# Kernel tuning notes

Hardware: AMD Instinct MI355X
Metric: run time of the kernel (lower is better)

The kernel has to match this reference:

```python
import jax, jax.numpy as jnp
import numpy as np

N_NODES = 100000


def gcn_conv(x, W, b, edge_index, n):
    # GCNConv: x' = D^{-1/2}(A+I)D^{-1/2} (x W) + b  (self-loops added, symmetric norm)
    h = x @ W                                  # [n, out]
    loop = jnp.arange(n, dtype=edge_index.dtype)
    row = jnp.concatenate([edge_index[0], loop])
    col = jnp.concatenate([edge_index[1], loop])
    deg = jax.ops.segment_sum(jnp.ones(col.shape, h.dtype), col, num_segments=n)
    dinv = jnp.where(deg > 0, jax.lax.rsqrt(deg), 0.0)
    norm = dinv[row] * dinv[col]               # [E+n]
    out = jax.ops.segment_sum(norm[:, None] * h[row], col, num_segments=n)
    return out + b


def setup_inputs() -> dict:
    key = jax.random.key(0)
    k1, k2, k3, k4, k5 = jax.random.split(key, 5)
    N, F, H, O = N_NODES, 128, 64, 32
    E, EL = 3200000, 200000
    x = jax.random.normal(k1, (N, F), dtype=jnp.float32)
    W1 = jax.random.normal(k2, (F, H), dtype=jnp.float32) * (1.0 / np.sqrt(F))
    b1 = jnp.zeros((H,), dtype=jnp.float32)
    W2 = jax.random.normal(k3, (H, O), dtype=jnp.float32) * (1.0 / np.sqrt(H))
    b2 = jnp.zeros((O,), dtype=jnp.float32)
    edge_index = jax.random.randint(k4, (2, E), 0, N, dtype=jnp.int64)
    edge_label_index = jax.random.randint(k5, (2, EL), 0, N, dtype=jnp.int64)
    return {"x": x, "W1": W1, "b1": b1, "W2": W2, "b2": b2,
            "edge_index": edge_index, "edge_label_index": edge_label_index}


def reference(x, W1, b1, W2, b2, edge_index, edge_label_index):
    n = x.shape[0]
    z = gcn_conv(x, W1, b1, edge_index, n)
    z = jax.nn.relu(z)
    z = gcn_conv(z, W2, b2, edge_index, n)     # [n, 32]
    # dot-product link decode
    return (z[edge_label_index[0]] * z[edge_label_index[1]]).sum(axis=1)
```

## Files before the change

kernel.cpp:

```cpp
#include <hip/hip_runtime.h>
#include <hip/hip_bf16.h>

typedef __hip_bfloat16 bf16;
typedef short s8v __attribute__((ext_vector_type(8)));
typedef float f4v __attribute__((ext_vector_type(4)));
typedef float v2f __attribute__((ext_vector_type(2)));

__device__ __forceinline__ short f2b(float f) {
  bf16 h = __float2bfloat16(f);
  return *reinterpret_cast<short*>(&h);
}
__device__ __forceinline__ void bf2_acc(int d, v2f& a) {
  v2f u;
  u.x = __int_as_float(d << 16);
  u.y = __int_as_float(d & 0xFFFF0000);
  a += u;
}

#define BSHIFT 8
#define BNODES 256
#define CHUNK 4096
#define SORT_CAP 12288
#define TSHIFT 15

__global__ __launch_bounds__(256) void k_hist(const int* __restrict__ col, int E,
                                              int nbuck, int* __restrict__ chist) {
  __shared__ int hist[512];
  int t = threadIdx.x;
  hist[t] = 0; hist[t + 256] = 0;
  __syncthreads();
  int e0 = blockIdx.x * CHUNK;
#pragma unroll
  for (int i = 0; i < 16; i++) {
    int e = e0 + i * 256 + t;
    if (e < E) atomicAdd(&hist[col[e] >> BSHIFT], 1);
  }
  __syncthreads();
  int* out = chist + (size_t)blockIdx.x * nbuck;
  for (int b = t; b < nbuck; b += 256) out[b] = hist[b];
}

__global__ __launch_bounds__(256) void k_scanbuck(int* __restrict__ chist, int nchnk,
                                                  int nbuck, int* __restrict__ btot) {
  __shared__ int sm[256];
  int b = blockIdx.x, t = threadIdx.x;
  int per = (nchnk + 255) / 256;
  int lo = t * per, hi = min(lo + per, nchnk);
  int s = 0;
  for (int i = lo; i < hi; i++) s += chist[(size_t)i * nbuck + b];
  sm[t] = s;
  __syncthreads();
  for (int d = 1; d < 256; d <<= 1) {
    int x = (t >= d) ? sm[t - d] : 0;
    __syncthreads();
    sm[t] += x;
    __syncthreads();
  }
  int off = (t == 0) ? 0 : sm[t - 1];
  for (int i = lo; i < hi; i++) {
    int c = chist[(size_t)i * nbuck + b];
    chist[(size_t)i * nbuck + b] = off;
    off += c;
  }
  if (t == 255) btot[b] = sm[255];
}

__global__ __launch_bounds__(512) void k_scanbase(const int* __restrict__ btot, int nbuck,
                                                  int* __restrict__ bbase,
                                                  int* __restrict__ row_start, int n) {
  __shared__ int sm[512];
  int t = threadIdx.x;
  int v = (t < nbuck) ? btot[t] : 0;
  sm[t] = v;
  __syncthreads();
  for (int d = 1; d < 512; d <<= 1) {
    int x = (t >= d) ? sm[t - d] : 0;
    __syncthreads();
    sm[t] += x;
    __syncthreads();
  }
  if (t < nbuck) bbase[t] = sm[t] - v;
  if (t == nbuck - 1) {
    bbase[nbuck] = sm[t];
    row_start[n] = sm[t];
  }
}

__global__ __launch_bounds__(256) void k_binpass(const int* __restrict__ row,
                                                 const int* __restrict__ col, int E,
                                                 int nbuck,
                                                 const int* __restrict__ bbase,
                                                 const int* __restrict__ chist,
                                                 int* __restrict__ adjTmp) {
  __shared__ int hist[512];
  __shared__ int base[512];
  __shared__ int lcur[512];
  __shared__ int gbase[512];
  __shared__ int psum[256];
  __shared__ int stage[CHUNK];
  __shared__ unsigned short sbkt[CHUNK];
  __shared__ int s_total;
  int t = threadIdx.x;
  int e0 = blockIdx.x * CHUNK;

  hist[t] = 0; hist[t + 256] = 0;
  __syncthreads();

  int pk[16], bk[16];
#pragma unroll
  for (int i = 0; i < 16; i++) {
    int e = e0 + i * 256 + t;
    if (e < E) {
      int c = col[e];
      int r = row[e];
      bk[i] = c >> BSHIFT;
      pk[i] = r | ((c & (BNODES - 1)) << 17);
      atomicAdd(&hist[bk[i]], 1);
    } else bk[i] = -1;
  }
  __syncthreads();
  int a0 = hist[2 * t], a1 = hist[2 * t + 1];
  psum[t] = a0 + a1;
  __syncthreads();
  for (int d = 1; d < 256; d <<= 1) {
    int v = (t >= d) ? psum[t - d] : 0;
    __syncthreads();
    psum[t] += v;
    __syncthreads();
  }
  int pref = (t == 0) ? 0 : psum[t - 1];
  base[2 * t] = pref;          lcur[2 * t] = pref;
  base[2 * t + 1] = pref + a0; lcur[2 * t + 1] = pref + a0;
  if (t == 255) s_total = psum[255];
  const int* coff = chist + (size_t)blockIdx.x * nbuck;
  for (int b = t; b < nbuck; b += 256) gbase[b] = bbase[b] + coff[b];
  __syncthreads();
#pragma unroll
  for (int i = 0; i < 16; i++) {
    if (bk[i] >= 0) {
      int pos = atomicAdd(&lcur[bk[i]], 1);
      stage[pos] = pk[i];
      sbkt[pos] = (unsigned short)bk[i];
    }
  }
  __syncthreads();
  int total = s_total;
  for (int i = t; i < total; i += 256) {
    int b = sbkt[i];
    adjTmp[gbase[b] + (i - base[b])] = stage[i];
  }
}

__global__ __launch_bounds__(256) void k_bucketsort(const int* __restrict__ bbase,
                                                    const int* __restrict__ adjTmp,
                                                    int* __restrict__ adj,
                                                    int* __restrict__ row_start,
                                                    float* __restrict__ dinv, int n) {
  __shared__ int cnt[1024];
  __shared__ int sc[256];
  __shared__ int cur[1024];
  __shared__ int stage[SORT_CAP];
  int b = blockIdx.x, t = threadIdx.x;
  int node_base = b << BSHIFT;
  int nnode = min(BNODES, n - node_base);
  int seg_base = bbase[b];
  int cntE = bbase[b + 1] - seg_base;
  cnt[t] = 0; cnt[t + 256] = 0; cnt[t + 512] = 0; cnt[t + 768] = 0;
  __syncthreads();
  for (int i = t; i < cntE; i += 256) {
    int p = adjTmp[seg_base + i];
    int key = (((p >> 17) & 255) << 2) | ((p >> TSHIFT) & 3);
    atomicAdd(&cnt[key], 1);
  }
  __syncthreads();
  int c0 = cnt[4 * t], c1 = cnt[4 * t + 1], c2 = cnt[4 * t + 2], c3 = cnt[4 * t + 3];
  int myc = c0 + c1 + c2 + c3;
  sc[t] = myc;
  __syncthreads();
  for (int d = 1; d < 256; d <<= 1) {
    int x = (t >= d) ? sc[t - d] : 0;
    __syncthreads();
    sc[t] += x;
    __syncthreads();
  }
  int excl = (t == 0) ? 0 : sc[t - 1];
  cur[4 * t] = excl;
  cur[4 * t + 1] = excl + c0;
  cur[4 * t + 2] = excl + c0 + c1;
  cur[4 * t + 3] = excl + c0 + c1 + c2;
  if (t < nnode) {
    row_start[node_base + t] = seg_base + excl;
    dinv[node_base + t] = rsqrtf((float)myc + 1.0f);
  }
  __syncthreads();
  if (cntE <= SORT_CAP) {
    for (int i = t; i < cntE; i += 256) {
      int p = adjTmp[seg_base + i];
      int key = (((p >> 17) & 255) << 2) | ((p >> TSHIFT) & 3);
      int pos = atomicAdd(&cur[key], 1);
      stage[pos] = (p & 0x1FFFF) << 7;
    }
    __syncthreads();
    for (int i = t; i < cntE; i += 256) adj[seg_base + i] = stage[i];
  } else {
    for (int i = t; i < cntE; i += 256) {
      int p = adjTmp[seg_base + i];
      int key = (((p >> 17) & 255) << 2) | ((p >> TSHIFT) & 3);
      int pos = atomicAdd(&cur[key], 1);
      adj[seg_base + pos] = (p & 0x1FFFF) << 7;
    }
  }
}

__global__ __launch_bounds__(256) void k_prepW(const float* __restrict__ W1,
                                               const float* __restrict__ W2,
                                               short* __restrict__ Wt1,
                                               short* __restrict__ Wt2) {
  int t = blockIdx.x * 256 + threadIdx.x;
  if (t < 128 * 64) { int k = t >> 6, c = t & 63; Wt1[c * 128 + k] = f2b(W1[t]); }
  if (t < 64 * 32)  { int k = t >> 5, c = t & 31; Wt2[c * 64 + k] = f2b(W2[t]); }
}

__global__ __launch_bounds__(256) void k_gemm1(const float* __restrict__ x,
                                               const short* __restrict__ Wt,
                                               const float* __restrict__ dinv,
                                               bf16* __restrict__ g1, int n) {
  int wave = threadIdx.x >> 6;
  int lane = threadIdx.x & 63;
  int m = lane & 15;
  int quad = lane >> 4;
  int r = blockIdx.x * 64 + wave * 16 + m;

  s8v afr[4];
  if (r < n) {
    const float* ap = x + (size_t)r * 128 + quad * 8;
#pragma unroll
    for (int kc = 0; kc < 4; kc++) {
      float4 u = *(const float4*)(ap + kc * 32);
      float4 v = *(const float4*)(ap + kc * 32 + 4);
      s8v a;
      a[0] = f2b(u.x); a[1] = f2b(u.y); a[2] = f2b(u.z); a[3] = f2b(u.w);
      a[4] = f2b(v.x); a[5] = f2b(v.y); a[6] = f2b(v.z); a[7] = f2b(v.w);
      afr[kc] = a;
    }
  } else {
#pragma unroll
    for (int kc = 0; kc < 4; kc++) afr[kc] = (s8v)(short)0;
  }

  const short* wp = Wt + (size_t)m * 128 + quad * 8;
  s8v bfr[4][4];
#pragma unroll
  for (int nt = 0; nt < 4; nt++)
#pragma unroll
    for (int kc = 0; kc < 4; kc++)
      bfr[nt][kc] = *(const s8v*)(wp + nt * 16 * 128 + kc * 32);

  f4v acc[4] = {f4v{0,0,0,0}, f4v{0,0,0,0}, f4v{0,0,0,0}, f4v{0,0,0,0}};
#pragma unroll
  for (int kc = 0; kc < 4; kc++)
#pragma unroll
    for (int nt = 0; nt < 4; nt++)
      acc[nt] = __builtin_amdgcn_mfma_f32_16x16x32_bf16(afr[kc], bfr[nt][kc], acc[nt], 0, 0, 0);

  int rbase = blockIdx.x * 64 + wave * 16 + quad * 4;
#pragma unroll
  for (int reg = 0; reg < 4; reg++) {
    int rr = rbase + reg;
    if (rr < n) {
      float dv = dinv[rr];
#pragma unroll
      for (int nt = 0; nt < 4; nt++)
        g1[(size_t)rr * 64 + nt * 16 + m] = __float2bfloat16(acc[nt][reg] * dv);
    }
  }
}

__global__ __launch_bounds__(256) void k_gemm2(const bf16* __restrict__ z1b,
                                               const short* __restrict__ Wt,
                                               const float* __restrict__ dinv,
                                               short* __restrict__ g2, int n) {
  int wave = threadIdx.x >> 6;
  int lane = threadIdx.x & 63;
  int m = lane & 15;
  int quad = lane >> 4;
  int r = blockIdx.x * 64 + wave * 16 + m;

  s8v afr[2];
  if (r < n) {
    const short* ap = (const short*)z1b + (size_t)r * 64 + quad * 8;
#pragma unroll
    for (int kc = 0; kc < 2; kc++) afr[kc] = *(const s8v*)(ap + kc * 32);
  } else {
#pragma unroll
    for (int kc = 0; kc < 2; kc++) afr[kc] = (s8v)(short)0;
  }

  const short* wp = Wt + (size_t)m * 64 + quad * 8;
  s8v bfr[2][2];
#pragma unroll
  for (int nt = 0; nt < 2; nt++)
#pragma unroll
    for (int kc = 0; kc < 2; kc++)
      bfr[nt][kc] = *(const s8v*)(wp + nt * 16 * 64 + kc * 32);

  f4v acc[2] = {f4v{0,0,0,0}, f4v{0,0,0,0}};
#pragma unroll
  for (int kc = 0; kc < 2; kc++)
#pragma unroll
    for (int nt = 0; nt < 2; nt++)
      acc[nt] = __builtin_amdgcn_mfma_f32_16x16x32_bf16(afr[kc], bfr[nt][kc], acc[nt], 0, 0, 0);

  int rbase = blockIdx.x * 64 + wave * 16 + quad * 4;
#pragma unroll
  for (int reg = 0; reg < 4; reg++) {
    int rr = rbase + reg;
    if (rr < n) {
      float dv = dinv[rr];
#pragma unroll
      for (int nt = 0; nt < 2; nt++)
        g2[(size_t)rr * 32 + nt * 16 + m] = f2b(acc[nt][reg] * dv);
    }
  }
}

__global__ __launch_bounds__(256) void k_gagg1(const int* __restrict__ row_start,
                                               const int* __restrict__ adj,
                                               const float* __restrict__ dinv,
                                               const short* __restrict__ g,
                                               const float* __restrict__ bias,
                                               short* __restrict__ z, int n, int E) {
  int wv = __builtin_amdgcn_readfirstlane((int)threadIdx.x) >> 6;
  int lane = threadIdx.x & 63;
  int grp = lane >> 3;
  int fl = lane & 7;
  int c0 = (blockIdx.x * 4 + wv) * 2;
  if (c0 >= n) return;
  int c1 = c0 + 1;
  bool hasB = (c1 < n);
  int sA = row_start[c0];
  int eA = row_start[c1];
  int eB = hasB ? row_start[c1 + 1] : eA;
  int sB = eA;
  const char* gb = (const char*)g;
  int fo = fl * 16;

  int mA = max(min(eA - 1, E - 1), 0);
  int mB = max(min(eB - 1, E - 1), 0);

  int vA0 = adj[min(sA + grp, mA)];
  int vA1 = adj[min(sA + 8 + grp, mA)];
  int vA2 = adj[min(sA + 16 + grp, mA)];
  int vA3 = adj[min(sA + 24 + grp, mA)];
  int vB0 = adj[min(sB + grp, mB)];
  int vB1 = adj[min(sB + 8 + grp, mB)];
  int vB2 = adj[min(sB + 16 + grp, mB)];
  int vB3 = adj[min(sB + 24 + grp, mB)];
  int4 p0 = *(const int4*)(gb + (unsigned)(vA0 + fo));
  int4 p1 = *(const int4*)(gb + (unsigned)(vA1 + fo));
  int4 p2 = *(const int4*)(gb + (unsigned)(vA2 + fo));
  int4 p3 = *(const int4*)(gb + (unsigned)(vA3 + fo));
  int4 q0 = *(const int4*)(gb + (unsigned)(vB0 + fo));
  int4 q1 = *(const int4*)(gb + (unsigned)(vB1 + fo));
  int4 q2 = *(const int4*)(gb + (unsigned)(vB2 + fo));
  int4 q3 = *(const int4*)(gb + (unsigned)(vB3 + fo));

  v2f a0 = {0.f, 0.f}, a1 = {0.f, 0.f}, a2 = {0.f, 0.f}, a3 = {0.f, 0.f};

  auto rest_row = [&](int j, int end) {
    for (; j + 32 <= end; j += 32) {
#pragma unroll
      for (int u = 0; u < 4; u++) {
        int voff = adj[j + u * 8 + grp];
        int4 pk = *(const int4*)(gb + (unsigned)(voff + fo));
        bf2_acc(pk.x, a0); bf2_acc(pk.y, a1); bf2_acc(pk.z, a2); bf2_acc(pk.w, a3);
      }
    }
    if (j < end) {
      int m = end - 1;
      int x0 = adj[min(j + grp, m)];
      int x1 = adj[min(j + 8 + grp, m)];
      int x2 = adj[min(j + 16 + grp, m)];
      int x3 = adj[min(j + 24 + grp, m)];
      int4 t0 = *(const int4*)(gb + (unsigned)(x0 + fo));
      int4 t1 = *(const int4*)(gb + (unsigned)(x1 + fo));
      int4 t2 = *(const int4*)(gb + (unsigned)(x2 + fo));
      int4 t3 = *(const int4*)(gb + (unsigned)(x3 + fo));
      if (j + grp < end)      { bf2_acc(t0.x, a0); bf2_acc(t0.y, a1); bf2_acc(t0.z, a2); bf2_acc(t0.w, a3); }
      if (j + 8 + grp < end)  { bf2_acc(t1.x, a0); bf2_acc(t1.y, a1); bf2_acc(t1.z, a2); bf2_acc(t1.w, a3); }
      if (j + 16 + grp < end) { bf2_acc(t2.x, a0); bf2_acc(t2.y, a1); bf2_acc(t2.z, a2); bf2_acc(t2.w, a3); }
      if (j + 24 + grp < end) { bf2_acc(t3.x, a0); bf2_acc(t3.y, a1); bf2_acc(t3.z, a2); bf2_acc(t3.w, a3); }
    }
  };

  auto finish = [&](int c) {
#pragma unroll
    for (int s = 8; s <= 32; s <<= 1) {
      a0.x += __shfl_xor(a0.x, s); a0.y += __shfl_xor(a0.y, s);
      a1.x += __shfl_xor(a1.x, s); a1.y += __shfl_xor(a1.y, s);
      a2.x += __shfl_xor(a2.x, s); a2.y += __shfl_xor(a2.y, s);
      a3.x += __shfl_xor(a3.x, s); a3.y += __shfl_xor(a3.y, s);
    }
    if (grp == 0) {
      int4 pk = *(const int4*)(gb + (((unsigned)c << 7) + fo));
      bf2_acc(pk.x, a0); bf2_acc(pk.y, a1);
      bf2_acc(pk.z, a2); bf2_acc(pk.w, a3);
      float d = dinv[c];
      float4 b0 = *(const float4*)(bias + fl * 8);
      float4 b1 = *(const float4*)(bias + fl * 8 + 4);
      float v0 = fmaxf(fmaf(d, a0.x, b0.x), 0.f);
      float v1 = fmaxf(fmaf(d, a0.y, b0.y), 0.f);
      float v2 = fmaxf(fmaf(d, a1.x, b0.z), 0.f);
      float v3 = fmaxf(fmaf(d, a1.y, b0.w), 0.f);
      float v4 = fmaxf(fmaf(d, a2.x, b1.x), 0.f);
      float v5 = fmaxf(fmaf(d, a2.y, b1.y), 0.f);
      float v6 = fmaxf(fmaf(d, a3.x, b1.z), 0.f);
      float v7 = fmaxf(fmaf(d, a3.y, b1.w), 0.f);
      int4 out;
      out.x = (int)(unsigned short)f2b(v0) | ((int)f2b(v1) << 16);
      out.y = (int)(unsigned short)f2b(v2) | ((int)f2b(v3) << 16);
      out.z = (int)(unsigned short)f2b(v4) | ((int)f2b(v5) << 16);
      out.w = (int)(unsigned short)f2b(v6) | ((int)f2b(v7) << 16);
      *(int4*)(z + c * 64 + fl * 8) = out;
    }
  };

  if (sA + grp < eA)      { bf2_acc(p0.x, a0); bf2_acc(p0.y, a1); bf2_acc(p0.z, a2); bf2_acc(p0.w, a3); }
  if (sA + 8 + grp < eA)  { bf2_acc(p1.x, a0); bf2_acc(p1.y, a1); bf2_acc(p1.z, a2); bf2_acc(p1.w, a3); }
  if (sA + 16 + grp < eA) { bf2_acc(p2.x, a0); bf2_acc(p2.y, a1); bf2_acc(p2.z, a2); bf2_acc(p2.w, a3); }
  if (sA + 24 + grp < eA) { bf2_acc(p3.x, a0); bf2_acc(p3.y, a1); bf2_acc(p3.z, a2); bf2_acc(p3.w, a3); }
  rest_row(sA + 32, eA);
  finish(c0);

  if (hasB) {
    a0 = v2f{0.f, 0.f}; a1 = v2f{0.f, 0.f}; a2 = v2f{0.f, 0.f}; a3 = v2f{0.f, 0.f};
    if (sB + grp < eB)      { bf2_acc(q0.x, a0); bf2_acc(q0.y, a1); bf2_acc(q0.z, a2); bf2_acc(q0.w, a3); }
    if (sB + 8 + grp < eB)  { bf2_acc(q1.x, a0); bf2_acc(q1.y, a1); bf2_acc(q1.z, a2); bf2_acc(q1.w, a3); }
    if (sB + 16 + grp < eB) { bf2_acc(q2.x, a0); bf2_acc(q2.y, a1); bf2_acc(q2.z, a2); bf2_acc(q2.w, a3); }
    if (sB + 24 + grp < eB) { bf2_acc(q3.x, a0); bf2_acc(q3.y, a1); bf2_acc(q3.z, a2); bf2_acc(q3.w, a3); }
    rest_row(sB + 32, eB);
    finish(c1);
  }
}

__global__ __launch_bounds__(256) void k_gagg2(const int* __restrict__ row_start,
                                               const int* __restrict__ adj,
                                               const float* __restrict__ dinv,
                                               const short* __restrict__ g,
                                               const float* __restrict__ bias,
                                               float* __restrict__ z, int n, int E) {
  int wv = __builtin_amdgcn_readfirstlane((int)threadIdx.x) >> 6;
  int lane = threadIdx.x & 63;
  int grp = lane >> 2;
  int fl = lane & 3;
  int c0 = (blockIdx.x * 4 + wv) * 2;
  if (c0 >= n) return;
  int c1 = c0 + 1;
  bool hasB = (c1 < n);
  int sA = row_start[c0];
  int eA = row_start[c1];
  int eB = hasB ? row_start[c1 + 1] : eA;
  int sB = eA;
  const char* gb = (const char*)g;
  int fo = fl * 16;

  int mA = max(min(eA - 1, E - 1), 0);
  int mB = max(min(eB - 1, E - 1), 0);

  int vA0 = adj[min(sA + grp, mA)];
  int vA1 = adj[min(sA + 16 + grp, mA)];
  int vB0 = adj[min(sB + grp, mB)];
  int vB1 = adj[min(sB + 16 + grp, mB)];
  int4 p0 = *(const int4*)(gb + (unsigned)((vA0 >> 1) + fo));
  int4 p1 = *(const int4*)(gb + (unsigned)((vA1 >> 1) + fo));
  int4 q0 = *(const int4*)(gb + (unsigned)((vB0 >> 1) + fo));
  int4 q1 = *(const int4*)(gb + (unsigned)((vB1 >> 1) + fo));

  v2f a0 = {0.f, 0.f}, a1 = {0.f, 0.f}, a2 = {0.f, 0.f}, a3 = {0.f, 0.f};

  auto rest_row = [&](int j, int end) {
    for (; j + 32 <= end; j += 32) {
#pragma unroll
      for (int u = 0; u < 2; u++) {
        int voff = adj[j + u * 16 + grp] >> 1;
        int4 pk = *(const int4*)(gb + (unsigned)(voff + fo));
        bf2_acc(pk.x, a0); bf2_acc(pk.y, a1); bf2_acc(pk.z, a2); bf2_acc(pk.w, a3);
      }
    }
    if (j < end) {
      int m = end - 1;
      int x0 = adj[min(j + grp, m)] >> 1;
      int x1 = adj[min(j + 16 + grp, m)] >> 1;
      int4 t0 = *(const int4*)(gb + (unsigned)(x0 + fo));
      int4 t1 = *(const int4*)(gb + (unsigned)(x1 + fo));
      if (j + grp < end)      { bf2_acc(t0.x, a0); bf2_acc(t0.y, a1); bf2_acc(t0.z, a2); bf2_acc(t0.w, a3); }
      if (j + 16 + grp < end) { bf2_acc(t1.x, a0); bf2_acc(t1.y, a1); bf2_acc(t1.z, a2); bf2_acc(t1.w, a3); }
    }
  };

  auto finish = [&](int c) {
#pragma unroll
    for (int s = 4; s <= 32; s <<= 1) {
      a0.x += __shfl_xor(a0.x, s); a0.y += __shfl_xor(a0.y, s);
      a1.x += __shfl_xor(a1.x, s); a1.y += __shfl_xor(a1.y, s);
      a2.x += __shfl_xor(a2.x, s); a2.y += __shfl_xor(a2.y, s);
      a3.x += __shfl_xor(a3.x, s); a3.y += __shfl_xor(a3.y, s);
    }
    if (grp == 0) {
      int4 pk = *(const int4*)(gb + (((unsigned)c << 6) + fo));
      bf2_acc(pk.x, a0); bf2_acc(pk.y, a1);
      bf2_acc(pk.z, a2); bf2_acc(pk.w, a3);
      float d = dinv[c];
      float4 b0 = *(const float4*)(bias + fl * 8);
      float4 b1 = *(const float4*)(bias + fl * 8 + 4);
      float4 o0, o1;
      o0.x = fmaf(d, a0.x, b0.x); o0.y = fmaf(d, a0.y, b0.y);
      o0.z = fmaf(d, a1.x, b0.z); o0.w = fmaf(d, a1.y, b0.w);
      o1.x = fmaf(d, a2.x, b1.x); o1.y = fmaf(d, a2.y, b1.y);
      o1.z = fmaf(d, a3.x, b1.z); o1.w = fmaf(d, a3.y, b1.w);
      *(float4*)(z + c * 32 + fl * 8) = o0;
      *(float4*)(z + c * 32 + fl * 8 + 4) = o1;
    }
  };

  if (sA + grp < eA)      { bf2_acc(p0.x, a0); bf2_acc(p0.y, a1); bf2_acc(p0.z, a2); bf2_acc(p0.w, a3); }
  if (sA + 16 + grp < eA) { bf2_acc(p1.x, a0); bf2_acc(p1.y, a1); bf2_acc(p1.z, a2); bf2_acc(p1.w, a3); }
  rest_row(sA + 32, eA);
  finish(c0);

  if (hasB) {
    a0 = v2f{0.f, 0.f}; a1 = v2f{0.f, 0.f}; a2 = v2f{0.f, 0.f}; a3 = v2f{0.f, 0.f};
    if (sB + grp < eB)      { bf2_acc(q0.x, a0); bf2_acc(q0.y, a1); bf2_acc(q0.z, a2); bf2_acc(q0.w, a3); }
    if (sB + 16 + grp < eB) { bf2_acc(q1.x, a0); bf2_acc(q1.y, a1); bf2_acc(q1.z, a2); bf2_acc(q1.w, a3); }
    rest_row(sB + 32, eB);
    finish(c1);
  }
}

__global__ __launch_bounds__(256) void k_decode(const int* __restrict__ ea,
                                                const int* __restrict__ eb,
                                                const float* __restrict__ z2,
                                                float* __restrict__ out, int EL) {
  int lane = threadIdx.x & 31;
  int e = blockIdx.x * 8 + (threadIdx.x >> 5);
  if (e >= EL) return;
  int a = ea[e], b = eb[e];
  float p = z2[a * 32 + lane] * z2[b * 32 + lane];
  p += __shfl_down(p, 16);
  p += __shfl_down(p, 8);
  p += __shfl_down(p, 4);
  p += __shfl_down(p, 2);
  p += __shfl_down(p, 1);
  if (lane == 0) out[e] = p;
}

extern "C" void kernel_launch(void* const* d_in, const int* in_sizes, int n_in,
                              void* d_out, int out_size, void* d_ws, size_t ws_size,
                              hipStream_t stream) {
  const float* x   = (const float*)d_in[0];
  const float* W1  = (const float*)d_in[1];
  const float* b1  = (const float*)d_in[2];
  const float* W2  = (const float*)d_in[3];
  const float* b2  = (const float*)d_in[4];
  const int*   ei  = (const int*)d_in[5];
  const int*   eli = (const int*)d_in[6];

  const int N  = in_sizes[0] / 128;
  const int E  = in_sizes[5] / 2;
  const int EL = in_sizes[6] / 2;
  const int* row = ei;
  const int* col = ei + E;
  const int NBUCK = (N + BNODES - 1) / BNODES;
  const int NCHNK = (E + CHUNK - 1) / CHUNK;

  char* ws = (char*)d_ws;
  size_t off = 0;
  auto take = [&](size_t bytes) { char* p = ws + off; off += (bytes + 255) & ~(size_t)255; return p; };
  float* dinv      = (float*)take((size_t)N * 4);
  int*   row_start = (int*)take((size_t)(N + 1) * 4);
  int*   btot      = (int*)take((size_t)NBUCK * 4);
  int*   bbase     = (int*)take((size_t)(NBUCK + 1) * 4);
  short* Wt1       = (short*)take((size_t)64 * 128 * 2);
  short* Wt2       = (short*)take((size_t)32 * 64 * 2);
  int*   chist     = (int*)take((size_t)NCHNK * NBUCK * 4);
  int*   adjTmp    = (int*)take((size_t)E * 4);
  int*   adj       = (int*)take((size_t)E * 4);
  char*  bufH      = take((size_t)N * 64 * 2);
  short* z1b       = (short*)take((size_t)N * 64 * 2);
  float* z2        = (float*)take((size_t)N * 32 * 4);
  (void)ws_size; (void)n_in; (void)out_size;

  bf16*  g1 = (bf16*)bufH;
  short* g2 = (short*)bufH;

  k_prepW     <<<32, 256, 0, stream>>>(W1, W2, Wt1, Wt2);
  k_hist      <<<NCHNK, 256, 0, stream>>>(col, E, NBUCK, chist);
  k_scanbuck  <<<NBUCK, 256, 0, stream>>>(chist, NCHNK, NBUCK, btot);
  k_scanbase  <<<1, 512, 0, stream>>>(btot, NBUCK, bbase, row_start, N);
  k_binpass   <<<NCHNK, 256, 0, stream>>>(row, col, E, NBUCK, bbase, chist, adjTmp);
  k_bucketsort<<<NBUCK, 256, 0, stream>>>(bbase, adjTmp, adj, row_start, dinv, N);

  k_gemm1<<<(N + 63) / 64, 256, 0, stream>>>(x, Wt1, dinv, g1, N);
  k_gagg1<<<(N + 7) / 8, 256, 0, stream>>>(row_start, adj, dinv, (const short*)g1, b1, z1b, N, E);

  k_gemm2<<<(N + 63) / 64, 256, 0, stream>>>((const bf16*)z1b, Wt2, dinv, g2, N);
  k_gagg2<<<(N + 7) / 8, 256, 0, stream>>>(row_start, adj, dinv, g2, b2, z2, N, E);

  k_decode<<<(EL + 7) / 8, 256, 0, stream>>>(eli, eli + EL, z2, (float*)d_out, EL);
}
```

Measured before the change: 303.1 us.

## Halve sort bucket width and stage layer-2 adjacency segments in LDS

```diff
diff --git a/kernel.cpp b/kernel.cpp
--- a/kernel.cpp
+++ b/kernel.cpp
@@ -17,17 +17,19 @@
   a += u;
 }
 
-#define BSHIFT 8
-#define BNODES 256
+#define BSHIFT 7
+#define BNODES 128
 #define CHUNK 4096
-#define SORT_CAP 12288
+#define SORT_CAP 6144
 #define TSHIFT 15
+#define NBMAX 1024
+#define ACAP 768
 
 __global__ __launch_bounds__(256) void k_hist(const int* __restrict__ col, int E,
                                               int nbuck, int* __restrict__ chist) {
-  __shared__ int hist[512];
+  __shared__ int hist[NBMAX];
   int t = threadIdx.x;
-  hist[t] = 0; hist[t + 256] = 0;
+  hist[t] = 0; hist[t + 256] = 0; hist[t + 512] = 0; hist[t + 768] = 0;
   __syncthreads();
   int e0 = blockIdx.x * CHUNK;
 #pragma unroll
@@ -70,8 +72,13 @@
                                                   int* __restrict__ row_start, int n) {
   __shared__ int sm[512];
   int t = threadIdx.x;
-  int v = (t < nbuck) ? btot[t] : 0;
-  sm[t] = v;
+  int b0 = 4 * t;
+  int v0 = (b0     < nbuck) ? btot[b0]     : 0;
+  int v1 = (b0 + 1 < nbuck) ? btot[b0 + 1] : 0;
+  int v2 = (b0 + 2 < nbuck) ? btot[b0 + 2] : 0;
+  int v3 = (b0 + 3 < nbuck) ? btot[b0 + 3] : 0;
+  int s = v0 + v1 + v2 + v3;
+  sm[t] = s;
   __syncthreads();
   for (int d = 1; d < 512; d <<= 1) {
     int x = (t >= d) ? sm[t - d] : 0;
@@ -79,10 +86,14 @@
     sm[t] += x;
     __syncthreads();
   }
-  if (t < nbuck) bbase[t] = sm[t] - v;
-  if (t == nbuck - 1) {
-    bbase[nbuck] = sm[t];
-    row_start[n] = sm[t];
+  int off = sm[t] - s;
+  if (b0     < nbuck) bbase[b0]     = off;
+  if (b0 + 1 < nbuck) bbase[b0 + 1] = off + v0;
+  if (b0 + 2 < nbuck) bbase[b0 + 2] = off + v0 + v1;
+  if (b0 + 3 < nbuck) bbase[b0 + 3] = off + v0 + v1 + v2;
+  if (t == 511) {
+    bbase[nbuck] = sm[511];
+    row_start[n] = sm[511];
   }
 }
 
@@ -92,10 +103,10 @@
                                                  const int* __restrict__ bbase,
                                                  const int* __restrict__ chist,
                                                  int* __restrict__ adjTmp) {
-  __shared__ int hist[512];
-  __shared__ int base[512];
-  __shared__ int lcur[512];
-  __shared__ int gbase[512];
+  __shared__ int hist[NBMAX];
+  __shared__ int base[NBMAX];
+  __shared__ int lcur[NBMAX];
+  __shared__ int gbase[NBMAX];
   __shared__ int psum[256];
   __shared__ int stage[CHUNK];
   __shared__ unsigned short sbkt[CHUNK];
@@ -103,7 +114,7 @@
   int t = threadIdx.x;
   int e0 = blockIdx.x * CHUNK;
 
-  hist[t] = 0; hist[t + 256] = 0;
+  for (int b = t; b < nbuck; b += 256) hist[b] = 0;
   __syncthreads();
 
   int pk[16], bk[16];
@@ -119,8 +130,11 @@
     } else bk[i] = -1;
   }
   __syncthreads();
-  int a0 = hist[2 * t], a1 = hist[2 * t + 1];
-  psum[t] = a0 + a1;
+  int PB = (nbuck + 255) >> 8;
+  int b0 = t * PB;
+  int s = 0;
+  for (int i = 0; i < PB; i++) { int b = b0 + i; if (b < nbuck) s += hist[b]; }
+  psum[t] = s;
   __syncthreads();
   for (int d = 1; d < 256; d <<= 1) {
     int v = (t >= d) ? psum[t - d] : 0;
@@ -128,9 +142,11 @@
     psum[t] += v;
     __syncthreads();
   }
-  int pref = (t == 0) ? 0 : psum[t - 1];
-  base[2 * t] = pref;          lcur[2 * t] = pref;
-  base[2 * t + 1] = pref + a0; lcur[2 * t + 1] = pref + a0;
+  int off = psum[t] - s;
+  for (int i = 0; i < PB; i++) {
+    int b = b0 + i;
+    if (b < nbuck) { base[b] = off; lcur[b] = off; off += hist[b]; }
+  }
   if (t == 255) s_total = psum[255];
   const int* coff = chist + (size_t)blockIdx.x * nbuck;
   for (int b = t; b < nbuck; b += 256) gbase[b] = bbase[b] + coff[b];
@@ -449,92 +465,110 @@
                                                const short* __restrict__ g,
                                                const float* __restrict__ bias,
                                                float* __restrict__ z, int n, int E) {
-  int wv = __builtin_amdgcn_readfirstlane((int)threadIdx.x) >> 6;
-  int lane = threadIdx.x & 63;
+  __shared__ int la[ACAP];
+  int t = threadIdx.x;
+  int cbase = blockIdx.x * 8;
+  int segLo = row_start[cbase];
+  int segHi = row_start[min(cbase + 8, n)];
+  int len = segHi - segLo;
+  bool fits = (len <= ACAP);
+  if (fits) {
+    for (int i = t; i < len; i += 256) la[i] = adj[segLo + i];
+    if (t == 0 && len == 0) la[0] = 0;
+  }
+  __syncthreads();
+
+  int wv = __builtin_amdgcn_readfirstlane(t) >> 6;
+  int lane = t & 63;
   int grp = lane >> 2;
   int fl = lane & 3;
-  int c0 = (blockIdx.x * 4 + wv) * 2;
+  int c0 = cbase + wv * 2;
   if (c0 >= n) return;
   int c1 = c0 + 1;
   bool hasB = (c1 < n);
   int sA = row_start[c0];
-  int eA = row_start[c1];
+  int eA = row_start[c0 + 1];
   int eB = hasB ? row_start[c1 + 1] : eA;
   int sB = eA;
   const char* gb = (const char*)g;
   int fo = fl * 16;
 
-  int mA = max(min(eA - 1, E - 1), 0);
-  int mB = max(min(eB - 1, E - 1), 0);
-
-  int vA0 = adj[min(sA + grp, mA)];
-  int vA1 = adj[min(sA + 16 + grp, mA)];
-  int vB0 = adj[min(sB + grp, mB)];
-  int vB1 = adj[min(sB + 16 + grp, mB)];
-  int4 p0 = *(const int4*)(gb + (unsigned)((vA0 >> 1) + fo));
-  int4 p1 = *(const int4*)(gb + (unsigned)((vA1 >> 1) + fo));
-  int4 q0 = *(const int4*)(gb + (unsigned)((vB0 >> 1) + fo));
-  int4 q1 = *(const int4*)(gb + (unsigned)((vB1 >> 1) + fo));
-
-  v2f a0 = {0.f, 0.f}, a1 = {0.f, 0.f}, a2 = {0.f, 0.f}, a3 = {0.f, 0.f};
-
-  auto rest_row = [&](int j, int end) {
-    for (; j + 32 <= end; j += 32) {
-#pragma unroll
-      for (int u = 0; u < 2; u++) {
-        int voff = adj[j + u * 16 + grp] >> 1;
-        int4 pk = *(const int4*)(gb + (unsigned)(voff + fo));
-        bf2_acc(pk.x, a0); bf2_acc(pk.y, a1); bf2_acc(pk.z, a2); bf2_acc(pk.w, a3);
+  int mA = max(min(eA - 1, E - 1), segLo);
+  int mB = max(min(eB - 1, E - 1), segLo);
+
+  auto run = [&](auto LD) {
+    int vA0 = LD(min(sA + grp, mA));
+    int vA1 = LD(min(sA + 16 + grp, mA));
+    int vB0 = LD(min(sB + grp, mB));
+    int vB1 = LD(min(sB + 16 + grp, mB));
+    int4 p0 = *(const int4*)(gb + (unsigned)((vA0 >> 1) + fo));
+    int4 p1 = *(const int4*)(gb + (unsigned)((vA1 >> 1) + fo));
+    int4 q0 = *(const int4*)(gb + (unsigned)((vB0 >> 1) + fo));
+    int4 q1 = *(const int4*)(gb + (unsigned)((vB1 >> 1) + fo));
+
+    v2f a0 = {0.f, 0.f}, a1 = {0.f, 0.f}, a2 = {0.f, 0.f}, a3 = {0.f, 0.f};
+
+    auto rest_row = [&](int j, int end) {
+      for (; j + 32 <= end; j += 32) {
+#pragma unroll
+        for (int u = 0; u < 2; u++) {
+          int voff = LD(j + u * 16 + grp) >> 1;
+          int4 pk = *(const int4*)(gb + (unsigned)(voff + fo));
+          bf2_acc(pk.x, a0); bf2_acc(pk.y, a1); bf2_acc(pk.z, a2); bf2_acc(pk.w, a3);
+        }
       }
-    }
-    if (j < end) {
-      int m = end - 1;
-      int x0 = adj[min(j + grp, m)] >> 1;
-      int x1 = adj[min(j + 16 + grp, m)] >> 1;
-      int4 t0 = *(const int4*)(gb + (unsigned)(x0 + fo));
-      int4 t1 = *(const int4*)(gb + (unsigned)(x1 + fo));
-      if (j + grp < end)      { bf2_acc(t0.x, a0); bf2_acc(t0.y, a1); bf2_acc(t0.z, a2); bf2_acc(t0.w, a3); }
-      if (j + 16 + grp < end) { bf2_acc(t1.x, a0); bf2_acc(t1.y, a1); bf2_acc(t1.z, a2); bf2_acc(t1.w, a3); }
+      if (j < end) {
+        int m = end - 1;
+        int x0 = LD(min(j + grp, m)) >> 1;
+        int x1 = LD(min(j + 16 + grp, m)) >> 1;
+        int4 t0 = *(const int4*)(gb + (unsigned)(x0 + fo));
+        int4 t1 = *(const int4*)(gb + (unsigned)(x1 + fo));
+        if (j + grp < end)      { bf2_acc(t0.x, a0); bf2_acc(t0.y, a1); bf2_acc(t0.z, a2); bf2_acc(t0.w, a3); }
+        if (j + 16 + grp < end) { bf2_acc(t1.x, a0); bf2_acc(t1.y, a1); bf2_acc(t1.z, a2); bf2_acc(t1.w, a3); }
+      }
+    };
+
+    auto finish = [&](int c) {
+#pragma unroll
+      for (int s = 4; s <= 32; s <<= 1) {
+        a0.x += __shfl_xor(a0.x, s); a0.y += __shfl_xor(a0.y, s);
+        a1.x += __shfl_xor(a1.x, s); a1.y += __shfl_xor(a1.y, s);
+        a2.x += __shfl_xor(a2.x, s); a2.y += __shfl_xor(a2.y, s);
+        a3.x += __shfl_xor(a3.x, s); a3.y += __shfl_xor(a3.y, s);
+      }
+      if (grp == 0) {
+        int4 pk = *(const int4*)(gb + (((unsigned)c << 6) + fo));
+        bf2_acc(pk.x, a0); bf2_acc(pk.y, a1);
+        bf2_acc(pk.z, a2); bf2_acc(pk.w, a3);
+        float d = dinv[c];
+        float4 b0 = *(const float4*)(bias + fl * 8);
+        float4 b1 = *(const float4*)(bias + fl * 8 + 4);
+        float4 o0, o1;
+        o0.x = fmaf(d, a0.x, b0.x); o0.y = fmaf(d, a0.y, b0.y);
+        o0.z = fmaf(d, a1.x, b0.z); o0.w = fmaf(d, a1.y, b0.w);
+        o1.x = fmaf(d, a2.x, b1.x); o1.y = fmaf(d, a2.y, b1.y);
+        o1.z = fmaf(d, a3.x, b1.z); o1.w = fmaf(d, a3.y, b1.w);
+        *(float4*)(z + c * 32 + fl * 8) = o0;
+        *(float4*)(z + c * 32 + fl * 8 + 4) = o1;
+      }
+    };
+
+    if (sA + grp < eA)      { bf2_acc(p0.x, a0); bf2_acc(p0.y, a1); bf2_acc(p0.z, a2); bf2_acc(p0.w, a3); }
+    if (sA + 16 + grp < eA) { bf2_acc(p1.x, a0); bf2_acc(p1.y, a1); bf2_acc(p1.z, a2); bf2_acc(p1.w, a3); }
+    rest_row(sA + 32, eA);
+    finish(c0);
+
+    if (hasB) {
+      a0 = v2f{0.f, 0.f}; a1 = v2f{0.f, 0.f}; a2 = v2f{0.f, 0.f}; a3 = v2f{0.f, 0.f};
+      if (sB + grp < eB)      { bf2_acc(q0.x, a0); bf2_acc(q0.y, a1); bf2_acc(q0.z, a2); bf2_acc(q0.w, a3); }
+      if (sB + 16 + grp < eB) { bf2_acc(q1.x, a0); bf2_acc(q1.y, a1); bf2_acc(q1.z, a2); bf2_acc(q1.w, a3); }
+      rest_row(sB + 32, eB);
+      finish(c1);
     }
   };
 
-  auto finish = [&](int c) {
-#pragma unroll
-    for (int s = 4; s <= 32; s <<= 1) {
-      a0.x += __shfl_xor(a0.x, s); a0.y += __shfl_xor(a0.y, s);
-      a1.x += __shfl_xor(a1.x, s); a1.y += __shfl_xor(a1.y, s);
-      a2.x += __shfl_xor(a2.x, s); a2.y += __shfl_xor(a2.y, s);
-      a3.x += __shfl_xor(a3.x, s); a3.y += __shfl_xor(a3.y, s);
-    }
-    if (grp == 0) {
-      int4 pk = *(const int4*)(gb + (((unsigned)c << 6) + fo));
-      bf2_acc(pk.x, a0); bf2_acc(pk.y, a1);
-      bf2_acc(pk.z, a2); bf2_acc(pk.w, a3);
-      float d = dinv[c];
-      float4 b0 = *(const float4*)(bias + fl * 8);
-      float4 b1 = *(const float4*)(bias + fl * 8 + 4);
-      float4 o0, o1;
-      o0.x = fmaf(d, a0.x, b0.x); o0.y = fmaf(d, a0.y, b0.y);
-      o0.z = fmaf(d, a1.x, b0.z); o0.w = fmaf(d, a1.y, b0.w);
-      o1.x = fmaf(d, a2.x, b1.x); o1.y = fmaf(d, a2.y, b1.y);
-      o1.z = fmaf(d, a3.x, b1.z); o1.w = fmaf(d, a3.y, b1.w);
-      *(float4*)(z + c * 32 + fl * 8) = o0;
-      *(float4*)(z + c * 32 + fl * 8 + 4) = o1;
-    }
-  };
-
-  if (sA + grp < eA)      { bf2_acc(p0.x, a0); bf2_acc(p0.y, a1); bf2_acc(p0.z, a2); bf2_acc(p0.w, a3); }
-  if (sA + 16 + grp < eA) { bf2_acc(p1.x, a0); bf2_acc(p1.y, a1); bf2_acc(p1.z, a2); bf2_acc(p1.w, a3); }
-  rest_row(sA + 32, eA);
-  finish(c0);
-
-  if (hasB) {
-    a0 = v2f{0.f, 0.f}; a1 = v2f{0.f, 0.f}; a2 = v2f{0.f, 0.f}; a3 = v2f{0.f, 0.f};
-    if (sB + grp < eB)      { bf2_acc(q0.x, a0); bf2_acc(q0.y, a1); bf2_acc(q0.z, a2); bf2_acc(q0.w, a3); }
-    if (sB + 16 + grp < eB) { bf2_acc(q1.x, a0); bf2_acc(q1.y, a1); bf2_acc(q1.z, a2); bf2_acc(q1.w, a3); }
-    rest_row(sB + 32, eB);
-    finish(c1);
-  }
+  if (fits) run([&](int i) { return la[i - segLo]; });
+  else      run([&](int i) { return adj[i]; });
 }
 
 __global__ __launch_bounds__(256) void k_decode(const int* __restrict__ ea,
```

New measurement: 314.3 us. 1.04x slower.

## Replace per-chunk histogram scan with atomic bucket cursors; stage adjacency in LDS for gagg2

Applied to the files above, without the earlier changes.

```diff
diff --git a/kernel.cpp b/kernel.cpp
--- a/kernel.cpp
+++ b/kernel.cpp
@@ -22,9 +22,21 @@
 #define CHUNK 4096
 #define SORT_CAP 12288
 #define TSHIFT 15
-
-__global__ __launch_bounds__(256) void k_hist(const int* __restrict__ col, int E,
-                                              int nbuck, int* __restrict__ chist) {
+#define ACAP 768
+
+__global__ __launch_bounds__(256) void k_prepW(const float* __restrict__ W1,
+                                               const float* __restrict__ W2,
+                                               short* __restrict__ Wt1,
+                                               short* __restrict__ Wt2,
+                                               int* __restrict__ btot, int nbuck) {
+  int t = blockIdx.x * 256 + threadIdx.x;
+  if (t < 128 * 64) { int k = t >> 6, c = t & 63; Wt1[c * 128 + k] = f2b(W1[t]); }
+  if (t < 64 * 32)  { int k = t >> 5, c = t & 31; Wt2[c * 64 + k] = f2b(W2[t]); }
+  if (t < nbuck)    btot[t] = 0;
+}
+
+__global__ __launch_bounds__(256) void k_count(const int* __restrict__ col, int E,
+                                               int nbuck, int* __restrict__ btot) {
   __shared__ int hist[512];
   int t = threadIdx.x;
   hist[t] = 0; hist[t + 256] = 0;
@@ -36,37 +48,13 @@
     if (e < E) atomicAdd(&hist[col[e] >> BSHIFT], 1);
   }
   __syncthreads();
-  int* out = chist + (size_t)blockIdx.x * nbuck;
-  for (int b = t; b < nbuck; b += 256) out[b] = hist[b];
-}
-
-__global__ __launch_bounds__(256) void k_scanbuck(int* __restrict__ chist, int nchnk,
-                                                  int nbuck, int* __restrict__ btot) {
-  __shared__ int sm[256];
-  int b = blockIdx.x, t = threadIdx.x;
-  int per = (nchnk + 255) / 256;
-  int lo = t * per, hi = min(lo + per, nchnk);
-  int s = 0;
-  for (int i = lo; i < hi; i++) s += chist[(size_t)i * nbuck + b];
-  sm[t] = s;
-  __syncthreads();
-  for (int d = 1; d < 256; d <<= 1) {
-    int x = (t >= d) ? sm[t - d] : 0;
-    __syncthreads();
-    sm[t] += x;
-    __syncthreads();
-  }
-  int off = (t == 0) ? 0 : sm[t - 1];
-  for (int i = lo; i < hi; i++) {
-    int c = chist[(size_t)i * nbuck + b];
-    chist[(size_t)i * nbuck + b] = off;
-    off += c;
-  }
-  if (t == 255) btot[b] = sm[255];
+  for (int b = t; b < nbuck; b += 256)
+    if (hist[b]) atomicAdd(&btot[b], hist[b]);
 }
 
 __global__ __launch_bounds__(512) void k_scanbase(const int* __restrict__ btot, int nbuck,
                                                   int* __restrict__ bbase,
+                                                  int* __restrict__ gcur,
                                                   int* __restrict__ row_start, int n) {
   __shared__ int sm[512];
   int t = threadIdx.x;
@@ -79,7 +67,11 @@
     sm[t] += x;
     __syncthreads();
   }
-  if (t < nbuck) bbase[t] = sm[t] - v;
+  if (t < nbuck) {
+    int e = sm[t] - v;
+    bbase[t] = e;
+    gcur[t] = e;
+  }
   if (t == nbuck - 1) {
     bbase[nbuck] = sm[t];
     row_start[n] = sm[t];
@@ -89,8 +81,7 @@
 __global__ __launch_bounds__(256) void k_binpass(const int* __restrict__ row,
                                                  const int* __restrict__ col, int E,
                                                  int nbuck,
-                                                 const int* __restrict__ bbase,
-                                                 const int* __restrict__ chist,
+                                                 int* __restrict__ gcur,
                                                  int* __restrict__ adjTmp) {
   __shared__ int hist[512];
   __shared__ int base[512];
@@ -132,8 +123,8 @@
   base[2 * t] = pref;          lcur[2 * t] = pref;
   base[2 * t + 1] = pref + a0; lcur[2 * t + 1] = pref + a0;
   if (t == 255) s_total = psum[255];
-  const int* coff = chist + (size_t)blockIdx.x * nbuck;
-  for (int b = t; b < nbuck; b += 256) gbase[b] = bbase[b] + coff[b];
+  for (int b = t; b < nbuck; b += 256)
+    gbase[b] = hist[b] ? atomicAdd(&gcur[b], hist[b]) : 0;
   __syncthreads();
 #pragma unroll
   for (int i = 0; i < 16; i++) {
@@ -210,15 +201,6 @@
       adj[seg_base + pos] = (p & 0x1FFFF) << 7;
     }
   }
-}
-
-__global__ __launch_bounds__(256) void k_prepW(const float* __restrict__ W1,
-                                               const float* __restrict__ W2,
-                                               short* __restrict__ Wt1,
-                                               short* __restrict__ Wt2) {
-  int t = blockIdx.x * 256 + threadIdx.x;
-  if (t < 128 * 64) { int k = t >> 6, c = t & 63; Wt1[c * 128 + k] = f2b(W1[t]); }
-  if (t < 64 * 32)  { int k = t >> 5, c = t & 31; Wt2[c * 64 + k] = f2b(W2[t]); }
 }
 
 __global__ __launch_bounds__(256) void k_gemm1(const float* __restrict__ x,
@@ -449,92 +431,110 @@
                                                const short* __restrict__ g,
                                                const float* __restrict__ bias,
                                                float* __restrict__ z, int n, int E) {
-  int wv = __builtin_amdgcn_readfirstlane((int)threadIdx.x) >> 6;
-  int lane = threadIdx.x & 63;
+  __shared__ int la[ACAP];
+  int t = threadIdx.x;
+  int cbase = blockIdx.x * 8;
+  int segLo = row_start[cbase];
+  int segHi = row_start[min(cbase + 8, n)];
+  int len = segHi - segLo;
+  bool fits = (len <= ACAP);
+  if (fits) {
+    for (int i = t; i < len; i += 256) la[i] = adj[segLo + i];
+    if (t == 0 && len == 0) la[0] = 0;
+  }
+  __syncthreads();
+
+  int wv = __builtin_amdgcn_readfirstlane(t) >> 6;
+  int lane = t & 63;
   int grp = lane >> 2;
   int fl = lane & 3;
-  int c0 = (blockIdx.x * 4 + wv) * 2;
+  int c0 = cbase + wv * 2;
   if (c0 >= n) return;
   int c1 = c0 + 1;
   bool hasB = (c1 < n);
   int sA = row_start[c0];
-  int eA = row_start[c1];
+  int eA = row_start[c0 + 1];
   int eB = hasB ? row_start[c1 + 1] : eA;
   int sB = eA;
   const char* gb = (const char*)g;
   int fo = fl * 16;
 
-  int mA = max(min(eA - 1, E - 1), 0);
-  int mB = max(min(eB - 1, E - 1), 0);
-
-  int vA0 = adj[min(sA + grp, mA)];
-  int vA1 = adj[min(sA + 16 + grp, mA)];
-  int vB0 = adj[min(sB + grp, mB)];
-  int vB1 = adj[min(sB + 16 + grp, mB)];
-  int4 p0 = *(const int4*)(gb + (unsigned)((vA0 >> 1) + fo));
-  int4 p1 = *(const int4*)(gb + (unsigned)((vA1 >> 1) + fo));
-  int4 q0 = *(const int4*)(gb + (unsigned)((vB0 >> 1) + fo));
-  int4 q1 = *(const int4*)(gb + (unsigned)((vB1 >> 1) + fo));
-
-  v2f a0 = {0.f, 0.f}, a1 = {0.f, 0.f}, a2 = {0.f, 0.f}, a3 = {0.f, 0.f};
-
-  auto rest_row = [&](int j, int end) {
-    for (; j + 32 <= end; j += 32) {
-#pragma unroll
-      for (int u = 0; u < 2; u++) {
-        int voff = adj[j + u * 16 + grp] >> 1;
-        int4 pk = *(const int4*)(gb + (unsigned)(voff + fo));
-        bf2_acc(pk.x, a0); bf2_acc(pk.y, a1); bf2_acc(pk.z, a2); bf2_acc(pk.w, a3);
+  int mA = max(min(eA - 1, E - 1), segLo);
+  int mB = max(min(eB - 1, E - 1), segLo);
+
+  auto run = [&](auto LD) {
+    int vA0 = LD(min(sA + grp, mA));
+    int vA1 = LD(min(sA + 16 + grp, mA));
+    int vB0 = LD(min(sB + grp, mB));
+    int vB1 = LD(min(sB + 16 + grp, mB));
+    int4 p0 = *(const int4*)(gb + (unsigned)((vA0 >> 1) + fo));
+    int4 p1 = *(const int4*)(gb + (unsigned)((vA1 >> 1) + fo));
+    int4 q0 = *(const int4*)(gb + (unsigned)((vB0 >> 1) + fo));
+    int4 q1 = *(const int4*)(gb + (unsigned)((vB1 >> 1) + fo));
+
+    v2f a0 = {0.f, 0.f}, a1 = {0.f, 0.f}, a2 = {0.f, 0.f}, a3 = {0.f, 0.f};
+
+    auto rest_row = [&](int j, int end) {
+      for (; j + 32 <= end; j += 32) {
+#pragma unroll
+        for (int u = 0; u < 2; u++) {
+          int voff = LD(j + u * 16 + grp) >> 1;
+          int4 pk = *(const int4*)(gb + (unsigned)(voff + fo));
+          bf2_acc(pk.x, a0); bf2_acc(pk.y, a1); bf2_acc(pk.z, a2); bf2_acc(pk.w, a3);
+        }
       }
-    }
-    if (j < end) {
-      int m = end - 1;
-      int x0 = adj[min(j + grp, m)] >> 1;
-      int x1 = adj[min(j + 16 + grp, m)] >> 1;
-      int4 t0 = *(const int4*)(gb + (unsigned)(x0 + fo));
-      int4 t1 = *(const int4*)(gb + (unsigned)(x1 + fo));
-      if (j + grp < end)      { bf2_acc(t0.x, a0); bf2_acc(t0.y, a1); bf2_acc(t0.z, a2); bf2_acc(t0.w, a3); }
-      if (j + 16 + grp < end) { bf2_acc(t1.x, a0); bf2_acc(t1.y, a1); bf2_acc(t1.z, a2); bf2_acc(t1.w, a3); }
+      if (j < end) {
+        int m = end - 1;
+        int x0 = LD(min(j + grp, m)) >> 1;
+        int x1 = LD(min(j + 16 + grp, m)) >> 1;
+        int4 t0 = *(const int4*)(gb + (unsigned)(x0 + fo));
+        int4 t1 = *(const int4*)(gb + (unsigned)(x1 + fo));
+        if (j + grp < end)      { bf2_acc(t0.x, a0); bf2_acc(t0.y, a1); bf2_acc(t0.z, a2); bf2_acc(t0.w, a3); }
+        if (j + 16 + grp < end) { bf2_acc(t1.x, a0); bf2_acc(t1.y, a1); bf2_acc(t1.z, a2); bf2_acc(t1.w, a3); }
+      }
+    };
+
+    auto finish = [&](int c) {
+#pragma unroll
+      for (int s = 4; s <= 32; s <<= 1) {
+        a0.x += __shfl_xor(a0.x, s); a0.y += __shfl_xor(a0.y, s);
+        a1.x += __shfl_xor(a1.x, s); a1.y += __shfl_xor(a1.y, s);
+        a2.x += __shfl_xor(a2.x, s); a2.y += __shfl_xor(a2.y, s);
+        a3.x += __shfl_xor(a3.x, s); a3.y += __shfl_xor(a3.y, s);
+      }
+      if (grp == 0) {
+        int4 pk = *(const int4*)(gb + (((unsigned)c << 6) + fo));
+        bf2_acc(pk.x, a0); bf2_acc(pk.y, a1);
+        bf2_acc(pk.z, a2); bf2_acc(pk.w, a3);
+        float d = dinv[c];
+        float4 b0 = *(const float4*)(bias + fl * 8);
+        float4 b1 = *(const float4*)(bias + fl * 8 + 4);
+        float4 o0, o1;
+        o0.x = fmaf(d, a0.x, b0.x); o0.y = fmaf(d, a0.y, b0.y);
+        o0.z = fmaf(d, a1.x, b0.z); o0.w = fmaf(d, a1.y, b0.w);
+        o1.x = fmaf(d, a2.x, b1.x); o1.y = fmaf(d, a2.y, b1.y);
+        o1.z = fmaf(d, a3.x, b1.z); o1.w = fmaf(d, a3.y, b1.w);
+        *(float4*)(z + c * 32 + fl * 8) = o0;
+        *(float4*)(z + c * 32 + fl * 8 + 4) = o1;
+      }
+    };
+
+    if (sA + grp < eA)      { bf2_acc(p0.x, a0); bf2_acc(p0.y, a1); bf2_acc(p0.z, a2); bf2_acc(p0.w, a3); }
+    if (sA + 16 + grp < eA) { bf2_acc(p1.x, a0); bf2_acc(p1.y, a1); bf2_acc(p1.z, a2); bf2_acc(p1.w, a3); }
+    rest_row(sA + 32, eA);
+    finish(c0);
+
+    if (hasB) {
+      a0 = v2f{0.f, 0.f}; a1 = v2f{0.f, 0.f}; a2 = v2f{0.f, 0.f}; a3 = v2f{0.f, 0.f};
+      if (sB + grp < eB)      { bf2_acc(q0.x, a0); bf2_acc(q0.y, a1); bf2_acc(q0.z, a2); bf2_acc(q0.w, a3); }
+      if (sB + 16 + grp < eB) { bf2_acc(q1.x, a0); bf2_acc(q1.y, a1); bf2_acc(q1.z, a2); bf2_acc(q1.w, a3); }
+      rest_row(sB + 32, eB);
+      finish(c1);
     }
   };
 
-  auto finish = [&](int c) {
-#pragma unroll
-    for (int s = 4; s <= 32; s <<= 1) {
-      a0.x += __shfl_xor(a0.x, s); a0.y += __shfl_xor(a0.y, s);
-      a1.x += __shfl_xor(a1.x, s); a1.y += __shfl_xor(a1.y, s);
-      a2.x += __shfl_xor(a2.x, s); a2.y += __shfl_xor(a2.y, s);
-      a3.x += __shfl_xor(a3.x, s); a3.y += __shfl_xor(a3.y, s);
-    }
-    if (grp == 0) {
-      int4 pk = *(const int4*)(gb + (((unsigned)c << 6) + fo));
-      bf2_acc(pk.x, a0); bf2_acc(pk.y, a1);
-      bf2_acc(pk.z, a2); bf2_acc(pk.w, a3);
-      float d = dinv[c];
-      float4 b0 = *(const float4*)(bias + fl * 8);
-      float4 b1 = *(const float4*)(bias + fl * 8 + 4);
-      float4 o0, o1;
-      o0.x = fmaf(d, a0.x, b0.x); o0.y = fmaf(d, a0.y, b0.y);
-      o0.z = fmaf(d, a1.x, b0.z); o0.w = fmaf(d, a1.y, b0.w);
-      o1.x = fmaf(d, a2.x, b1.x); o1.y = fmaf(d, a2.y, b1.y);
-      o1.z = fmaf(d, a3.x, b1.z); o1.w = fmaf(d, a3.y, b1.w);
-      *(float4*)(z + c * 32 + fl * 8) = o0;
-      *(float4*)(z + c * 32 + fl * 8 + 4) = o1;
-    }
-  };
-
-  if (sA + grp < eA)      { bf2_acc(p0.x, a0); bf2_acc(p0.y, a1); bf2_acc(p0.z, a2); bf2_acc(p0.w, a3); }
-  if (sA + 16 + grp < eA) { bf2_acc(p1.x, a0); bf2_acc(p1.y, a1); bf2_acc(p1.z, a2); bf2_acc(p1.w, a3); }
-  rest_row(sA + 32, eA);
-  finish(c0);
-
-  if (hasB) {
-    a0 = v2f{0.f, 0.f}; a1 = v2f{0.f, 0.f}; a2 = v2f{0.f, 0.f}; a3 = v2f{0.f, 0.f};
-    if (sB + grp < eB)      { bf2_acc(q0.x, a0); bf2_acc(q0.y, a1); bf2_acc(q0.z, a2); bf2_acc(q0.w, a3); }
-    if (sB + 16 + grp < eB) { bf2_acc(q1.x, a0); bf2_acc(q1.y, a1); bf2_acc(q1.z, a2); bf2_acc(q1.w, a3); }
-    rest_row(sB + 32, eB);
-    finish(c1);
-  }
+  if (fits) run([&](int i) { return la[i - segLo]; });
+  else      run([&](int i) { return adj[i]; });
 }
 
 __global__ __launch_bounds__(256) void k_decode(const int* __restrict__ ea,
@@ -580,9 +580,9 @@
   int*   row_start = (int*)take((size_t)(N + 1) * 4);
   int*   btot      = (int*)take((size_t)NBUCK * 4);
   int*   bbase     = (int*)take((size_t)(NBUCK + 1) * 4);
+  int*   gcur      = (int*)take((size_t)NBUCK * 4);
   short* Wt1       = (short*)take((size_t)64 * 128 * 2);
   short* Wt2       = (short*)take((size_t)32 * 64 * 2);
-  int*   chist     = (int*)take((size_t)NCHNK * NBUCK * 4);
   int*   adjTmp    = (int*)take((size_t)E * 4);
   int*   adj       = (int*)take((size_t)E * 4);
   char*  bufH      = take((size_t)N * 64 * 2);
@@ -593,11 +593,10 @@
   bf16*  g1 = (bf16*)bufH;
   short* g2 = (short*)bufH;
 
-  k_prepW     <<<32, 256, 0, stream>>>(W1, W2, Wt1, Wt2);
-  k_hist      <<<NCHNK, 256, 0, stream>>>(col, E, NBUCK, chist);
-  k_scanbuck  <<<NBUCK, 256, 0, stream>>>(chist, NCHNK, NBUCK, btot);
-  k_scanbase  <<<1, 512, 0, stream>>>(btot, NBUCK, bbase, row_start, N);
-  k_binpass   <<<NCHNK, 256, 0, stream>>>(row, col, E, NBUCK, bbase, chist, adjTmp);
+  k_prepW     <<<32, 256, 0, stream>>>(W1, W2, Wt1, Wt2, btot, NBUCK);
+  k_count     <<<NCHNK, 256, 0, stream>>>(col, E, NBUCK, btot);
+  k_scanbase  <<<1, 512, 0, stream>>>(btot, NBUCK, bbase, gcur, row_start, N);
+  k_binpass   <<<NCHNK, 256, 0, stream>>>(row, col, E, NBUCK, gcur, adjTmp);
   k_bucketsort<<<NBUCK, 256, 0, stream>>>(bbase, adjTmp, adj, row_start, dinv, N);
 
   k_gemm1<<<(N + 63) / 64, 256, 0, stream>>>(x, Wt1, dinv, g1, N);
```

Measured after the change: 318.1 us. +4.9%, slower.
